# Kernel optimization log

Hardware: AMD Instinct MI355X
Metric: run time of the kernel (lower is better)

Reference implementation:

```python
import jax, jax.numpy as jnp
import numpy as np

N_NODES = 50000


def gcn_conv(x, src, dst, W, b, n):
    # PyG GCNConv: h = x @ W; add self-loops; sym-norm aggregate; + bias
    h = x @ W
    loop = jnp.arange(n, dtype=src.dtype)
    s = jnp.concatenate([src, loop])
    d = jnp.concatenate([dst, loop])
    deg = jax.ops.segment_sum(jnp.ones(s.shape[0], h.dtype), d, num_segments=n)
    dinv = jnp.where(deg > 0, jax.lax.rsqrt(deg), 0.0)
    norm = dinv[s] * dinv[d]  # [E+n]
    msg = h[s] * norm[:, None]  # [E+n, C] gather
    out = jax.ops.segment_sum(msg, d, num_segments=n)  # scatter-add
    return out + b


def mlp_decode(z, src, dst, Wa, ba, Wb, bb):
    feat = jnp.concatenate([z[src], z[dst]], axis=1)  # [P, 2*out]
    hid = jax.nn.relu(feat @ Wa + ba)
    return hid @ Wb + bb  # [P, 1]


def setup_inputs() -> dict:
    key = jax.random.key(0)
    ks = jax.random.split(key, 12)
    in_c, hid_c, out_c = 128, 128, 64
    E, P = 800000, 200000
    x = jax.random.normal(ks[0], (N_NODES, in_c), dtype=jnp.float32)
    edge_index = jax.random.randint(ks[1], (2, E), 0, N_NODES, dtype=jnp.int64)
    pos_edge_index = jax.random.randint(ks[2], (2, P), 0, N_NODES, dtype=jnp.int64)
    neg_edge_index = jax.random.randint(ks[3], (2, P), 0, N_NODES, dtype=jnp.int64)
    s1 = 1.0 / np.sqrt(in_c)
    s2 = 1.0 / np.sqrt(hid_c)
    s3 = 1.0 / np.sqrt(2 * out_c)
    W1 = jax.random.uniform(ks[4], (in_c, hid_c), jnp.float32, -s1, s1)
    b1 = jnp.zeros((hid_c,), jnp.float32)
    W2 = jax.random.uniform(ks[5], (hid_c, out_c), jnp.float32, -s2, s2)
    b2 = jnp.zeros((out_c,), jnp.float32)
    Wa = jax.random.uniform(ks[6], (2 * out_c, hid_c), jnp.float32, -s3, s3)
    ba = jax.random.uniform(ks[7], (hid_c,), jnp.float32, -s3, s3)
    Wb = jax.random.uniform(ks[8], (hid_c, 1), jnp.float32, -s2, s2)
    bb = jax.random.uniform(ks[9], (1,), jnp.float32, -s2, s2)
    return {"x": x, "edge_index": edge_index, "pos_edge_index": pos_edge_index,
            "neg_edge_index": neg_edge_index, "W1": W1, "b1": b1, "W2": W2,
            "b2": b2, "Wa": Wa, "ba": ba, "Wb": Wb, "bb": bb}


def reference(x, edge_index, pos_edge_index, neg_edge_index,
              W1, b1, W2, b2, Wa, ba, Wb, bb):
    src, dst = edge_index[0], edge_index[1]
    n = x.shape[0]
    z = gcn_conv(x, src, dst, W1, b1, n)
    z = jax.nn.relu(z)  # dropout disabled in eval mode
    z = gcn_conv(z, src, dst, W2, b2, n)
    pos_pred = mlp_decode(z, pos_edge_index[0], pos_edge_index[1], Wa, ba, Wb, bb)
    neg_pred = mlp_decode(z, neg_edge_index[0], neg_edge_index[1], Wa, ba, Wb, bb)
    return (pos_pred, neg_pred)
```

## Files before the change

kernel.cpp:

```cpp
#include <hip/hip_runtime.h>
#include <hip/hip_bf16.h>
#include <hip/hip_fp16.h>

#define NODES 50000
#define NEDGE 800000
#define NPRED 200000

typedef __attribute__((ext_vector_type(8))) short bf16x8;
typedef __attribute__((ext_vector_type(8))) unsigned short u16x8;
typedef __attribute__((ext_vector_type(4))) float f32x4;

__device__ inline float bf2f(unsigned short u) {
    union { unsigned int i; float f; } v; v.i = ((unsigned int)u) << 16; return v.f;
}
__device__ inline unsigned short f2bf(float f) {
    __hip_bfloat16 b = __float2bfloat16(f);
    return *(unsigned short*)&b;
}

__global__ __launch_bounds__(256) void rank_count4(const int* __restrict__ dstv, int* __restrict__ cnt,
                                                   int* __restrict__ rank, int E4) {
    int i = blockIdx.x * 256 + threadIdx.x;
    if (i < E4) {
        int4 d4 = ((const int4*)dstv)[i];
        int4 r4;
        r4.x = atomicAdd(&cnt[d4.x], 1);
        r4.y = atomicAdd(&cnt[d4.y], 1);
        r4.z = atomicAdd(&cnt[d4.z], 1);
        r4.w = atomicAdd(&cnt[d4.w], 1);
        ((int4*)rank)[i] = r4;
    }
}

__global__ __launch_bounds__(256) void scan_bsum(const int* __restrict__ cnt, int* __restrict__ bsum, int n) {
    __shared__ int s[256];
    int t = threadIdx.x, b = blockIdx.x;
    int base = b * 1024 + t * 4;
    int sum = 0;
#pragma unroll
    for (int j = 0; j < 4; ++j) { int i = base + j; if (i < n) sum += cnt[i]; }
    s[t] = sum; __syncthreads();
    for (int off = 128; off >= 1; off >>= 1) {
        if (t < off) s[t] += s[t + off];
        __syncthreads();
    }
    if (t == 0) bsum[b] = s[0];
}

__global__ void scan_boff(const int* __restrict__ bsum, int* __restrict__ boff, int nb,
                          int* __restrict__ row_ptr, int n) {
    int t = threadIdx.x;
    int v = (t < nb) ? bsum[t] : 0;
    int orig = v;
    for (int off = 1; off < 64; off <<= 1) {
        int u = __shfl_up(v, off, 64);
        if (t >= off) v += u;
    }
    boff[t] = v - orig;
    if (t == 63) row_ptr[n] = v;
}

__global__ __launch_bounds__(256) void scan_write(const int* __restrict__ cnt, const int* __restrict__ boff,
                                                  int* __restrict__ row_ptr, float* __restrict__ dinv, int n) {
    __shared__ int s[256];
    int t = threadIdx.x, b = blockIdx.x;
    int base = b * 1024 + t * 4;
    int v[4]; int sum = 0;
#pragma unroll
    for (int j = 0; j < 4; ++j) { int i = base + j; v[j] = (i < n) ? cnt[i] : 0; sum += v[j]; }
    s[t] = sum; __syncthreads();
    for (int off = 1; off < 256; off <<= 1) {
        int u = (t >= off) ? s[t - off] : 0;
        __syncthreads();
        s[t] += u;
        __syncthreads();
    }
    int run = s[t] - sum + boff[b];
#pragma unroll
    for (int j = 0; j < 4; ++j) {
        int i = base + j;
        if (i < n) {
            row_ptr[i] = run; run += v[j];
            dinv[i] = rsqrtf((float)(v[j] + 1));
        }
    }
}

__global__ __launch_bounds__(256) void csr_fill2(const int* __restrict__ ei, const int* __restrict__ rank,
                                                 const int* __restrict__ row_ptr, int* __restrict__ colv, int E4) {
    int i = blockIdx.x * 256 + threadIdx.x;
    if (i < E4) {
        int4 s4 = ((const int4*)ei)[i];
        int4 d4 = ((const int4*)(ei + NEDGE))[i];
        int4 r4 = ((const int4*)rank)[i];
        colv[row_ptr[d4.x] + r4.x] = s4.x;
        colv[row_ptr[d4.y] + r4.y] = s4.y;
        colv[row_ptr[d4.z] + r4.z] = s4.z;
        colv[row_ptr[d4.w] + r4.w] = s4.w;
    }
}

__global__ __launch_bounds__(256) void perm_all(const float* __restrict__ W1, const float* __restrict__ W2,
                                                const float* __restrict__ Wa,
                                                unsigned short* __restrict__ pW1,
                                                unsigned short* __restrict__ pW2,
                                                unsigned short* __restrict__ pWa) {
    int t = blockIdx.x * 256 + threadIdx.x;
    if (t >= 5120) return;
    const float* W; unsigned short* P; int N;
    if (t < 2048)      { W = W1; P = pW1; N = 128; }
    else if (t < 3072) { W = W2; P = pW2; N = 64;  t -= 2048; }
    else               { W = Wa; P = pWa; N = 128; t -= 3072; }
    int lane = t & 63;
    int kt = (t >> 6) & 3;
    int nt = t >> 8;
    int n = nt * 16 + (lane & 15);
    int k0 = kt * 32 + (lane >> 4) * 8;
#pragma unroll
    for (int j = 0; j < 8; ++j) P[t * 8 + j] = f2bf(W[(k0 + j) * N + n]);
}

template <int NT, bool AFP32>
__global__ __launch_bounds__(256) void gemm_mfma(const void* __restrict__ Xv,
                                                 const unsigned short* __restrict__ perm,
                                                 unsigned short* __restrict__ H, int M) {
    int w = blockIdx.x * 4 + (threadIdx.x >> 6);
    int m0 = w * 16;
    if (m0 >= M) return;
    int lane = threadIdx.x & 63;
    int m = lane & 15, q = lane >> 4;
    size_t row = (size_t)(m0 + m);
    bf16x8 a[4];
    if (AFP32) {
        const float* X = (const float*)Xv;
#pragma unroll
        for (int kt = 0; kt < 4; ++kt) {
            float4 f0 = *(const float4*)&X[row * 128 + kt * 32 + q * 8];
            float4 f1 = *(const float4*)&X[row * 128 + kt * 32 + q * 8 + 4];
            bf16x8 av;
            av[0] = (short)f2bf(f0.x); av[1] = (short)f2bf(f0.y);
            av[2] = (short)f2bf(f0.z); av[3] = (short)f2bf(f0.w);
            av[4] = (short)f2bf(f1.x); av[5] = (short)f2bf(f1.y);
            av[6] = (short)f2bf(f1.z); av[7] = (short)f2bf(f1.w);
            a[kt] = av;
        }
    } else {
        const unsigned short* X = (const unsigned short*)Xv;
#pragma unroll
        for (int kt = 0; kt < 4; ++kt)
            a[kt] = *(const bf16x8*)&X[row * 128 + kt * 32 + q * 8];
    }
    const int N = NT * 16;
#pragma unroll
    for (int nt = 0; nt < NT; ++nt) {
        f32x4 c = {0.f, 0.f, 0.f, 0.f};
#pragma unroll
        for (int kt = 0; kt < 4; ++kt) {
            bf16x8 b = *(const bf16x8*)(perm + (size_t)((nt * 4 + kt) * 64 + lane) * 8);
            c = __builtin_amdgcn_mfma_f32_16x16x32_bf16(a[kt], b, c, 0, 0, 0);
        }
#pragma unroll
        for (int r = 0; r < 4; ++r)
            H[(size_t)(m0 + q * 4 + r) * N + nt * 16 + m] = f2bf(c[r]);
    }
}

template <int C, bool RELU>
__global__ __launch_bounds__(256) void agg_bf16(const unsigned short* __restrict__ h,
                                                const int* __restrict__ row_ptr, const int* __restrict__ colv,
                                                const float* __restrict__ dinv, const float* __restrict__ bias,
                                                unsigned short* __restrict__ out) {
    constexpr int TPN = C / 8;
    constexpr int NPB = 256 / TPN;
    int d = blockIdx.x * NPB + threadIdx.x / TPN;
    if (d >= NODES) return;
    int c8 = (threadIdx.x % TPN) * 8;
    float dv = dinv[d];
    float acc[8];
    u16x8 self = *(const u16x8*)&h[(size_t)d * C + c8];
#pragma unroll
    for (int j = 0; j < 8; ++j) acc[j] = bf2f(self[j]) * dv;
    int i = row_ptr[d], end = row_ptr[d + 1];
    for (; i + 3 < end; i += 4) {
        int s0 = colv[i], s1 = colv[i + 1], s2 = colv[i + 2], s3 = colv[i + 3];
        float w0 = dinv[s0], w1 = dinv[s1], w2 = dinv[s2], w3 = dinv[s3];
        u16x8 r0 = *(const u16x8*)&h[(size_t)s0 * C + c8];
        u16x8 r1 = *(const u16x8*)&h[(size_t)s1 * C + c8];
        u16x8 r2 = *(const u16x8*)&h[(size_t)s2 * C + c8];
        u16x8 r3 = *(const u16x8*)&h[(size_t)s3 * C + c8];
#pragma unroll
        for (int j = 0; j < 8; ++j)
            acc[j] += bf2f(r0[j]) * w0 + bf2f(r1[j]) * w1 + bf2f(r2[j]) * w2 + bf2f(r3[j]) * w3;
    }
    for (; i < end; ++i) {
        int s0 = colv[i];
        float w0 = dinv[s0];
        u16x8 r0 = *(const u16x8*)&h[(size_t)s0 * C + c8];
#pragma unroll
        for (int j = 0; j < 8; ++j) acc[j] += bf2f(r0[j]) * w0;
    }
    u16x8 ov;
#pragma unroll
    for (int j = 0; j < 8; ++j) {
        float o = acc[j] * dv + bias[c8 + j];
        if (RELU) o = fmaxf(o, 0.f);
        ov[j] = f2bf(o);
    }
    *(u16x8*)&out[(size_t)d * C + c8] = ov;
}

__global__ __launch_bounds__(256) void decode_mfma2(const unsigned short* __restrict__ zb,
                                                    const int* __restrict__ pos, const int* __restrict__ neg,
                                                    const unsigned short* __restrict__ perm,
                                                    const float* __restrict__ ba, const float* __restrict__ Wb,
                                                    const float* __restrict__ bb, float* __restrict__ out, int P) {
    int lane = threadIdx.x & 63;
    int w = blockIdx.x * 4 + (threadIdx.x >> 6);
    int g0 = w * 4;
    if (g0 >= 12500) return;
    int m = lane & 15, q = lane >> 4;
    float bav[8], wbv[8];
#pragma unroll
    for (int nt = 0; nt < 8; ++nt) { bav[nt] = ba[nt * 16 + m]; wbv[nt] = Wb[nt * 16 + m]; }
    float bbv = bb[0];

    int idxS[3][2], idxD[3][2], base[3];
    bf16x8 A[2][8];

    auto loadIdx = [&](int it) {
        int slot = it % 3;
        int g = g0 + it;
        int half = (g >= 6250) ? 1 : 0;
        const int* src = half ? neg : pos;
        int e0 = (g - half * 6250) * 32;
        base[slot] = half * P + e0;
        int eA = e0 + m, eB = e0 + 16 + m;
        idxS[slot][0] = src[eA]; idxD[slot][0] = src[P + eA];
        idxS[slot][1] = src[eB]; idxD[slot][1] = src[P + eB];
    };
    auto loadFrags = [&](int it) {
        int slot = it % 3, buf = it & 1;
        size_t s0 = (size_t)idxS[slot][0] * 64, d0 = (size_t)idxD[slot][0] * 64;
        size_t s1 = (size_t)idxS[slot][1] * 64, d1 = (size_t)idxD[slot][1] * 64;
        A[buf][0] = *(const bf16x8*)(zb + s0 + q * 8);
        A[buf][1] = *(const bf16x8*)(zb + s0 + 32 + q * 8);
        A[buf][2] = *(const bf16x8*)(zb + d0 + q * 8);
        A[buf][3] = *(const bf16x8*)(zb + d0 + 32 + q * 8);
        A[buf][4] = *(const bf16x8*)(zb + s1 + q * 8);
        A[buf][5] = *(const bf16x8*)(zb + s1 + 32 + q * 8);
        A[buf][6] = *(const bf16x8*)(zb + d1 + q * 8);
        A[buf][7] = *(const bf16x8*)(zb + d1 + 32 + q * 8);
    };

    loadIdx(0); loadIdx(1); loadFrags(0);
#pragma unroll
    for (int it = 0; it < 4; ++it) {
        if (it + 2 < 4) loadIdx(it + 2);
        if (it + 1 < 4) loadFrags(it + 1);
        int buf = it & 1;
        float p0[4] = {0.f, 0.f, 0.f, 0.f};
        float p1[4] = {0.f, 0.f, 0.f, 0.f};
#pragma unroll
        for (int nt = 0; nt < 8; ++nt) {
            f32x4 c0 = {0.f, 0.f, 0.f, 0.f};
            f32x4 c1 = {0.f, 0.f, 0.f, 0.f};
#pragma unroll
            for (int kt = 0; kt < 4; ++kt) {
                bf16x8 b = *(const bf16x8*)(perm + (size_t)((nt * 4 + kt) * 64 + lane) * 8);
                c0 = __builtin_amdgcn_mfma_f32_16x16x32_bf16(A[buf][kt], b, c0, 0, 0, 0);
                c1 = __builtin_amdgcn_mfma_f32_16x16x32_bf16(A[buf][4 + kt], b, c1, 0, 0, 0);
            }
#pragma unroll
            for (int r = 0; r < 4; ++r) {
                p0[r] += fmaxf(c0[r] + bav[nt], 0.f) * wbv[nt];
                p1[r] += fmaxf(c1[r] + bav[nt], 0.f) * wbv[nt];
            }
        }
#pragma unroll
        for (int off = 1; off <= 8; off <<= 1) {
#pragma unroll
            for (int r = 0; r < 4; ++r) {
                p0[r] += __shfl_xor(p0[r], off, 64);
                p1[r] += __shfl_xor(p1[r], off, 64);
            }
        }
        if (m == 0) {
            int slot = it % 3;
            float4 st0 = { p0[0] + bbv, p0[1] + bbv, p0[2] + bbv, p0[3] + bbv };
            float4 st1 = { p1[0] + bbv, p1[1] + bbv, p1[2] + bbv, p1[3] + bbv };
            *(float4*)&out[base[slot] + q * 4] = st0;
            *(float4*)&out[base[slot] + 16 + q * 4] = st1;
        }
    }
}

extern "C" void kernel_launch(void* const* d_in, const int* in_sizes, int n_in,
                              void* d_out, int out_size, void* d_ws, size_t ws_size,
                              hipStream_t stream) {
    const int N = NODES, E = NEDGE, P = NPRED;
    const float* x  = (const float*)d_in[0];
    const int*   ei = (const int*)d_in[1];
    const int*  pos = (const int*)d_in[2];
    const int*  neg = (const int*)d_in[3];
    const float* W1 = (const float*)d_in[4];
    const float* b1 = (const float*)d_in[5];
    const float* W2 = (const float*)d_in[6];
    const float* b2 = (const float*)d_in[7];
    const float* Wa = (const float*)d_in[8];
    const float* ba = (const float*)d_in[9];
    const float* Wb = (const float*)d_in[10];
    const float* bb = (const float*)d_in[11];
    float* out = (float*)d_out;

    char* w = (char*)d_ws;
    auto alloc = [&](size_t bytes) { char* p = w; w += (bytes + 255) & ~(size_t)255; return p; };
    int*   cnt     = (int*)alloc((size_t)N * 4);
    int*   rankb   = (int*)alloc((size_t)E * 4);
    int*   row_ptr = (int*)alloc((size_t)(N + 1) * 4);
    int*   colv    = (int*)alloc((size_t)E * 4);
    float* dinv    = (float*)alloc((size_t)N * 4);
    int*   bsum    = (int*)alloc(64 * 4);
    int*   boff    = (int*)alloc(64 * 4);
    unsigned short* h1b = (unsigned short*)alloc((size_t)N * 128 * 2);
    unsigned short* z1b = (unsigned short*)alloc((size_t)N * 128 * 2);
    unsigned short* h2b = (unsigned short*)alloc((size_t)N * 64 * 2);
    unsigned short* zb  = (unsigned short*)alloc((size_t)N * 64 * 2);
    unsigned short* pW1 = (unsigned short*)alloc(2048 * 8 * 2);
    unsigned short* pW2 = (unsigned short*)alloc(1024 * 8 * 2);
    unsigned short* pWa = (unsigned short*)alloc(2048 * 8 * 2);

    const int nb = (N + 1023) / 1024;
    hipMemsetAsync(cnt, 0, (size_t)N * 4, stream);
    rank_count4<<<(E / 4 + 255) / 256, 256, 0, stream>>>(ei + E, cnt, rankb, E / 4);
    scan_bsum<<<nb, 256, 0, stream>>>(cnt, bsum, N);
    scan_boff<<<1, 64, 0, stream>>>(bsum, boff, nb, row_ptr, N);
    scan_write<<<nb, 256, 0, stream>>>(cnt, boff, row_ptr, dinv, N);
    csr_fill2<<<(E / 4 + 255) / 256, 256, 0, stream>>>(ei, rankb, row_ptr, colv, E / 4);

    perm_all<<<20, 256, 0, stream>>>(W1, W2, Wa, pW1, pW2, pWa);

    gemm_mfma<8, true><<<782, 256, 0, stream>>>(x, pW1, h1b, N);
    agg_bf16<128, true><<<N / 16, 256, 0, stream>>>(h1b, row_ptr, colv, dinv, b1, z1b);

    gemm_mfma<4, false><<<782, 256, 0, stream>>>(z1b, pW2, h2b, N);
    agg_bf16<64, false><<<(N + 31) / 32, 256, 0, stream>>>(h2b, row_ptr, colv, dinv, b2, zb);

    decode_mfma2<<<782, 256, 0, stream>>>(zb, pos, neg, pWa, ba, Wb, bb, out, P);
}
```

Before: 260.6 us.

## Stage decode weights in LDS and halve per-wave work in MLP decode

```diff
diff --git a/kernel.cpp b/kernel.cpp
--- a/kernel.cpp
+++ b/kernel.cpp
@@ -209,71 +209,78 @@
     *(u16x8*)&out[(size_t)d * C + c8] = ov;
 }
 
-__global__ __launch_bounds__(256) void decode_mfma2(const unsigned short* __restrict__ zb,
+__global__ __launch_bounds__(256) void decode_mfma3(const unsigned short* __restrict__ zb,
                                                     const int* __restrict__ pos, const int* __restrict__ neg,
                                                     const unsigned short* __restrict__ perm,
                                                     const float* __restrict__ ba, const float* __restrict__ Wb,
                                                     const float* __restrict__ bb, float* __restrict__ out, int P) {
-    int lane = threadIdx.x & 63;
-    int w = blockIdx.x * 4 + (threadIdx.x >> 6);
-    int g0 = w * 4;
-    if (g0 >= 12500) return;
+    __shared__ unsigned short sB[2048 * 8];
+    int tid = threadIdx.x;
+#pragma unroll
+    for (int i = tid * 8; i < 2048 * 8; i += 256 * 8)
+        *(u16x8*)&sB[i] = *(const u16x8*)&perm[i];
+    __syncthreads();
+
+    int w = blockIdx.x * 4 + (tid >> 6);
+    if (w >= 6250) return;
+    int lane = tid & 63;
     int m = lane & 15, q = lane >> 4;
     float bav[8], wbv[8];
 #pragma unroll
     for (int nt = 0; nt < 8; ++nt) { bav[nt] = ba[nt * 16 + m]; wbv[nt] = Wb[nt * 16 + m]; }
     float bbv = bb[0];
-
-    int idxS[3][2], idxD[3][2], base[3];
+    int g0 = w * 2;
+
+    int idxS[2][2], idxD[2][2], base[2];
     bf16x8 A[2][8];
-
     auto loadIdx = [&](int it) {
-        int slot = it % 3;
         int g = g0 + it;
         int half = (g >= 6250) ? 1 : 0;
         const int* src = half ? neg : pos;
         int e0 = (g - half * 6250) * 32;
-        base[slot] = half * P + e0;
-        int eA = e0 + m, eB = e0 + 16 + m;
-        idxS[slot][0] = src[eA]; idxD[slot][0] = src[P + eA];
-        idxS[slot][1] = src[eB]; idxD[slot][1] = src[P + eB];
+        base[it] = half * P + e0;
+        idxS[it][0] = src[e0 + m];      idxD[it][0] = src[P + e0 + m];
+        idxS[it][1] = src[e0 + 16 + m]; idxD[it][1] = src[P + e0 + 16 + m];
     };
-    auto loadFrags = [&](int it) {
-        int slot = it % 3, buf = it & 1;
-        size_t s0 = (size_t)idxS[slot][0] * 64, d0 = (size_t)idxD[slot][0] * 64;
-        size_t s1 = (size_t)idxS[slot][1] * 64, d1 = (size_t)idxD[slot][1] * 64;
-        A[buf][0] = *(const bf16x8*)(zb + s0 + q * 8);
-        A[buf][1] = *(const bf16x8*)(zb + s0 + 32 + q * 8);
-        A[buf][2] = *(const bf16x8*)(zb + d0 + q * 8);
-        A[buf][3] = *(const bf16x8*)(zb + d0 + 32 + q * 8);
-        A[buf][4] = *(const bf16x8*)(zb + s1 + q * 8);
-        A[buf][5] = *(const bf16x8*)(zb + s1 + 32 + q * 8);
-        A[buf][6] = *(const bf16x8*)(zb + d1 + q * 8);
-        A[buf][7] = *(const bf16x8*)(zb + d1 + 32 + q * 8);
+    auto loadA = [&](int it) {
+        size_t s0 = (size_t)idxS[it][0] * 64, d0 = (size_t)idxD[it][0] * 64;
+        size_t s1 = (size_t)idxS[it][1] * 64, d1 = (size_t)idxD[it][1] * 64;
+        A[it][0] = *(const bf16x8*)(zb + s0 + q * 8);
+        A[it][1] = *(const bf16x8*)(zb + s0 + 32 + q * 8);
+        A[it][2] = *(const bf16x8*)(zb + d0 + q * 8);
+        A[it][3] = *(const bf16x8*)(zb + d0 + 32 + q * 8);
+        A[it][4] = *(const bf16x8*)(zb + s1 + q * 8);
+        A[it][5] = *(const bf16x8*)(zb + s1 + 32 + q * 8);
+        A[it][6] = *(const bf16x8*)(zb + d1 + q * 8);
+        A[it][7] = *(const bf16x8*)(zb + d1 + 32 + q * 8);
     };
 
-    loadIdx(0); loadIdx(1); loadFrags(0);
-#pragma unroll
-    for (int it = 0; it < 4; ++it) {
-        if (it + 2 < 4) loadIdx(it + 2);
-        if (it + 1 < 4) loadFrags(it + 1);
-        int buf = it & 1;
+    loadIdx(0); loadIdx(1); loadA(0);
+#pragma unroll
+    for (int it = 0; it < 2; ++it) {
+        if (it + 1 < 2) loadA(it + 1);
         float p0[4] = {0.f, 0.f, 0.f, 0.f};
         float p1[4] = {0.f, 0.f, 0.f, 0.f};
 #pragma unroll
         for (int nt = 0; nt < 8; ++nt) {
-            f32x4 c0 = {0.f, 0.f, 0.f, 0.f};
-            f32x4 c1 = {0.f, 0.f, 0.f, 0.f};
-#pragma unroll
-            for (int kt = 0; kt < 4; ++kt) {
-                bf16x8 b = *(const bf16x8*)(perm + (size_t)((nt * 4 + kt) * 64 + lane) * 8);
-                c0 = __builtin_amdgcn_mfma_f32_16x16x32_bf16(A[buf][kt], b, c0, 0, 0, 0);
-                c1 = __builtin_amdgcn_mfma_f32_16x16x32_bf16(A[buf][4 + kt], b, c1, 0, 0, 0);
-            }
+            bf16x8 b0 = *(const bf16x8*)&sB[(size_t)((nt * 4 + 0) * 64 + lane) * 8];
+            bf16x8 b1 = *(const bf16x8*)&sB[(size_t)((nt * 4 + 1) * 64 + lane) * 8];
+            bf16x8 b2 = *(const bf16x8*)&sB[(size_t)((nt * 4 + 2) * 64 + lane) * 8];
+            bf16x8 b3 = *(const bf16x8*)&sB[(size_t)((nt * 4 + 3) * 64 + lane) * 8];
+            f32x4 c0a = {0.f, 0.f, 0.f, 0.f}, c0b = {0.f, 0.f, 0.f, 0.f};
+            f32x4 c1a = {0.f, 0.f, 0.f, 0.f}, c1b = {0.f, 0.f, 0.f, 0.f};
+            c0a = __builtin_amdgcn_mfma_f32_16x16x32_bf16(A[it][0], b0, c0a, 0, 0, 0);
+            c1a = __builtin_amdgcn_mfma_f32_16x16x32_bf16(A[it][4], b0, c1a, 0, 0, 0);
+            c0b = __builtin_amdgcn_mfma_f32_16x16x32_bf16(A[it][2], b2, c0b, 0, 0, 0);
+            c1b = __builtin_amdgcn_mfma_f32_16x16x32_bf16(A[it][6], b2, c1b, 0, 0, 0);
+            c0a = __builtin_amdgcn_mfma_f32_16x16x32_bf16(A[it][1], b1, c0a, 0, 0, 0);
+            c1a = __builtin_amdgcn_mfma_f32_16x16x32_bf16(A[it][5], b1, c1a, 0, 0, 0);
+            c0b = __builtin_amdgcn_mfma_f32_16x16x32_bf16(A[it][3], b3, c0b, 0, 0, 0);
+            c1b = __builtin_amdgcn_mfma_f32_16x16x32_bf16(A[it][7], b3, c1b, 0, 0, 0);
 #pragma unroll
             for (int r = 0; r < 4; ++r) {
-                p0[r] += fmaxf(c0[r] + bav[nt], 0.f) * wbv[nt];
-                p1[r] += fmaxf(c1[r] + bav[nt], 0.f) * wbv[nt];
+                p0[r] += fmaxf(c0a[r] + c0b[r] + bav[nt], 0.f) * wbv[nt];
+                p1[r] += fmaxf(c1a[r] + c1b[r] + bav[nt], 0.f) * wbv[nt];
             }
         }
 #pragma unroll
@@ -285,11 +292,10 @@
             }
         }
         if (m == 0) {
-            int slot = it % 3;
             float4 st0 = { p0[0] + bbv, p0[1] + bbv, p0[2] + bbv, p0[3] + bbv };
             float4 st1 = { p1[0] + bbv, p1[1] + bbv, p1[2] + bbv, p1[3] + bbv };
-            *(float4*)&out[base[slot] + q * 4] = st0;
-            *(float4*)&out[base[slot] + 16 + q * 4] = st1;
+            *(float4*)&out[base[it] + q * 4] = st0;
+            *(float4*)&out[base[it] + 16 + q * 4] = st1;
         }
     }
 }
@@ -345,5 +351,5 @@
     gemm_mfma<4, false><<<782, 256, 0, stream>>>(z1b, pW2, h2b, N);
     agg_bf16<64, false><<<(N + 31) / 32, 256, 0, stream>>>(h2b, row_ptr, colv, dinv, b2, zb);
 
-    decode_mfma2<<<782, 256, 0, stream>>>(zb, pos, neg, pWa, ba, Wb, bb, out, P);
-}
+    decode_mfma3<<<1563, 256, 0, stream>>>(zb, pos, neg, pWa, ba, Wb, bb, out, P);
+}
```

New measurement: 245.2 us. -5.9%, faster.
